# Kernel optimization log

Measured on AMD Instinct MI355X. Metric: run time of the kernel, lower is better.

The kernel has to match this reference:

```python
import jax, jax.numpy as jnp
import numpy as np

N_NODES = 100000
IN_CH, HID_CH, OUT_CH = 128, 128, 64
N_EDGES = 1600000


def setup_inputs() -> dict:
    key = jax.random.key(0)
    ks = jax.random.split(key, 6)
    x = jax.random.normal(ks[0], (N_NODES, IN_CH), dtype=jnp.float32)
    edge_index = jax.random.randint(ks[1], (2, N_EDGES), 0, N_NODES, dtype=jnp.int64)
    # Glorot-style init for GCNConv linear weights, zero bias (PyG defaults)
    s1 = (6.0 / (IN_CH + HID_CH)) ** 0.5
    s2 = (6.0 / (HID_CH + OUT_CH)) ** 0.5
    W1 = jax.random.uniform(ks[2], (IN_CH, HID_CH), jnp.float32, -s1, s1)
    b1 = jnp.zeros((HID_CH,), jnp.float32)
    W2 = jax.random.uniform(ks[3], (HID_CH, OUT_CH), jnp.float32, -s2, s2)
    b2 = jnp.zeros((OUT_CH,), jnp.float32)
    return {"x": x, "W1": W1, "b1": b1, "W2": W2, "b2": b2, "edge_index": edge_index}


def _gcn_norm(edge_index, num_nodes):
    # Add self-loops, compute symmetric normalization deg^{-1/2} A_hat deg^{-1/2}
    loop = jnp.arange(num_nodes, dtype=edge_index.dtype)
    row = jnp.concatenate([edge_index[0], loop])  # source
    col = jnp.concatenate([edge_index[1], loop])  # target
    deg = jax.ops.segment_sum(jnp.ones_like(col, dtype=jnp.float32), col,
                              num_segments=num_nodes)
    dinv = jnp.where(deg > 0, jax.lax.rsqrt(deg), 0.0)
    norm = dinv[row] * dinv[col]  # [E + N]
    return row, col, norm


def _gcn_conv(x, W, b, row, col, norm, num_nodes):
    h = x @ W                              # [N, C_out]
    msg = h[row] * norm[:, None]           # gather over sources, [E+N, C_out]
    out = jax.ops.segment_sum(msg, col, num_segments=num_nodes)  # scatter-add
    return out + b


def reference(x, W1, b1, W2, b2, edge_index):
    num_nodes = x.shape[0]
    row, col, norm = _gcn_norm(edge_index, num_nodes)
    # dropout(p=0.5) in eval mode is identity
    h = _gcn_conv(x, W1, b1, row, col, norm, num_nodes)
    h = jax.nn.relu(h)
    out = _gcn_conv(h, W2, b2, row, col, norm, num_nodes)
    return out
```

## Files before the change

### kernel.cpp

```cpp
#include <hip/hip_runtime.h>
#include <hip/hip_fp16.h>

typedef _Float16 half8 __attribute__((ext_vector_type(8)));
typedef float floatx4 __attribute__((ext_vector_type(4)));
typedef unsigned int uintx4 __attribute__((ext_vector_type(4)));


#define NBUK 128
#define CAPB 16384

__global__ __launch_bounds__(256) void bucket_kernel(const int* __restrict__ rows,
                                                     const int* __restrict__ cols,
                                                     int E, int NSUB,
                                                     int* __restrict__ bcur,
                                                     unsigned* __restrict__ bdata) {
    __shared__ int hcnt[NBUK];
    __shared__ int hbase[NBUK];
    const int tid = threadIdx.x;
    const int chunk0 = blockIdx.x * 2048;
    if (tid < NBUK) hcnt[tid] = 0;
    __syncthreads();
    unsigned up[8];
    int ub[8];
#pragma unroll
    for (int q = 0; q < 8; ++q) {
        int e = chunk0 + q * 256 + tid;
        ub[q] = -1;
        if (e < E) {
            unsigned r = (unsigned)rows[e];
            unsigned c = (unsigned)cols[e];
            int b = (int)(c / (unsigned)NSUB);
            unsigned lc = c - (unsigned)b * (unsigned)NSUB;
            ub[q] = b;
            up[q] = r | (lc << 17);
            atomicAdd(&hcnt[b], 1);
        }
    }
    __syncthreads();
    if (tid < NBUK) {
        hbase[tid] = atomicAdd(&bcur[tid], hcnt[tid]);
        hcnt[tid] = 0;
    }
    __syncthreads();
#pragma unroll
    for (int q = 0; q < 8; ++q) {
        if (ub[q] >= 0) {
            int idx = hbase[ub[q]] + atomicAdd(&hcnt[ub[q]], 1);
            if (idx < CAPB) bdata[(size_t)ub[q] * CAPB + idx] = up[q];
        }
    }
}

__global__ __launch_bounds__(128) void exscan_bucket_kernel(const int* __restrict__ bcur,
                                                            int* __restrict__ bbase,
                                                            int N, int* __restrict__ baseOut) {
    __shared__ int s[NBUK];
    int tid = threadIdx.x;
    int v = min(bcur[tid], CAPB);
    s[tid] = v;
    __syncthreads();
    for (int d = 1; d < NBUK; d <<= 1) {
        int t = (tid >= d) ? s[tid - d] : 0;
        __syncthreads();
        s[tid] += t;
        __syncthreads();
    }
    bbase[tid] = s[tid] - v;
    if (tid == NBUK - 1) baseOut[N] = s[tid];
}

__global__ __launch_bounds__(256) void sortfill_kernel(const unsigned* __restrict__ bdata,
                                                       const int* __restrict__ bcur,
                                                       const int* __restrict__ bbase,
                                                       int NSUB, int N,
                                                       int* __restrict__ baseOut,
                                                       float* __restrict__ dinvOut,
                                                       int* __restrict__ srcSorted) {
    __shared__ int cnt[1024];
    __shared__ int cur[1024];
    __shared__ int wsum[4];
    __shared__ int srcOut[CAPB];
    const int tid = threadIdx.x;
    const int b = blockIdx.x;
    const int nb = min(bcur[b], CAPB);
    const int base0 = bbase[b];
    const int n0 = b * NSUB;
    const int nn = min(NSUB, N - n0);
    const unsigned* bd = bdata + (size_t)b * CAPB;

    for (int i = tid; i < 1024; i += 256) cnt[i] = 0;
    __syncthreads();
    for (int i = tid; i < nb; i += 256) atomicAdd(&cnt[bd[i] >> 17], 1);
    __syncthreads();
    int a0 = cnt[4 * tid], a1 = cnt[4 * tid + 1], a2 = cnt[4 * tid + 2], a3 = cnt[4 * tid + 3];
    int s0 = a0, s1 = s0 + a1, s2 = s1 + a2, s3 = s2 + a3;
    int tot = s3;
    const int lane = tid & 63, wid = tid >> 6;
    for (int off = 1; off < 64; off <<= 1) {
        int u = __shfl_up(tot, off, 64);
        if (lane >= off) tot += u;
    }
    if (lane == 63) wsum[wid] = tot;
    __syncthreads();
    int woff = 0;
#pragma unroll
    for (int w = 0; w < 4; ++w)
        if (w < wid) woff += wsum[w];
    const int tbase = woff + tot - s3;
    cur[4 * tid]     = tbase;
    cur[4 * tid + 1] = tbase + s0;
    cur[4 * tid + 2] = tbase + s1;
    cur[4 * tid + 3] = tbase + s2;
    __syncthreads();
    for (int i = tid; i < nn; i += 256) {
        baseOut[n0 + i] = base0 + cur[i];
        dinvOut[n0 + i] = rsqrtf((float)cnt[i] + 1.0f);
    }
    __syncthreads();
    for (int i = tid; i < nb; i += 256) {
        unsigned u = bd[i];
        int c = (int)(u >> 17);
        int p = atomicAdd(&cur[c], 1);
        srcOut[p] = (int)(u & 0x1FFFFu);
    }
    __syncthreads();
    for (int i = tid; i < nb; i += 256) srcSorted[base0 + i] = srcOut[i];
}

__global__ __launch_bounds__(256) void wtrans_kernel(const float* __restrict__ W,
                                                     __half* __restrict__ WT, int C) {
    int idx = blockIdx.x * 256 + threadIdx.x;
    if (idx >= 128 * C) return;
    int k = idx / C, c = idx % C;
    float v = W[idx];
    WT[c * 128 + (k ^ ((c & 7) << 3))] = __float2half_rn(v);
}

template <int COLS, typename XT>
__global__ __launch_bounds__(256) void mfma_gemm(const XT* __restrict__ X,
                                                 const __half* __restrict__ WT,
                                                 const float* __restrict__ dinv,
                                                 __half* __restrict__ H, int N) {
    __shared__ _Float16 sX[64 * 128];
    __shared__ _Float16 sW[COLS * 128];
    const int tid = threadIdx.x;
    const int row0 = blockIdx.x * 64;

    {
        const uintx4* src = (const uintx4*)WT;
        uintx4* dst = (uintx4*)sW;
        for (int i = tid; i < COLS * 16; i += 256) dst[i] = src[i];
    }
    for (int cidx = tid; cidx < 1024; cidx += 256) {
        int r = cidx >> 4, k8 = cidx & 15;
        int gr = row0 + r;
        half8 h;
#pragma unroll
        for (int q = 0; q < 8; ++q) h[q] = (_Float16)0.f;
        if (gr < N) {
            if constexpr (sizeof(XT) == 4) {
                const float4* p = (const float4*)((const float*)X + (size_t)gr * 128 + k8 * 8);
                float4 f0 = p[0], f1 = p[1];
                h[0] = (_Float16)f0.x; h[1] = (_Float16)f0.y;
                h[2] = (_Float16)f0.z; h[3] = (_Float16)f0.w;
                h[4] = (_Float16)f1.x; h[5] = (_Float16)f1.y;
                h[6] = (_Float16)f1.z; h[7] = (_Float16)f1.w;
            } else {
                h = *(const half8*)((const _Float16*)X + (size_t)gr * 128 + k8 * 8);
            }
        }
        *(half8*)(sX + r * 128 + ((k8 * 8) ^ ((r & 7) << 3))) = h;
    }
    __syncthreads();

    const int w = tid >> 6;
    const int lane = tid & 63;
    const int l15 = lane & 15, l4 = lane >> 4;
    constexpr int WCOLS = COLS / 2;
    constexpr int NCB = WCOLS / 16;
    const int wr = (w >> 1) * 32;
    const int wc = (w & 1) * WCOLS;

    half8 a[2][4];
#pragma unroll
    for (int rb = 0; rb < 2; ++rb) {
        int r = wr + rb * 16 + l15;
#pragma unroll
        for (int kb = 0; kb < 4; ++kb)
            a[rb][kb] = *(const half8*)(sX + r * 128 + ((kb * 32 + l4 * 8) ^ ((r & 7) << 3)));
    }

    floatx4 acc[2][NCB];
#pragma unroll
    for (int rb = 0; rb < 2; ++rb)
#pragma unroll
        for (int cb = 0; cb < NCB; ++cb) acc[rb][cb] = (floatx4)(0.f);

#pragma unroll
    for (int cb = 0; cb < NCB; ++cb) {
        int c = wc + cb * 16 + l15;
#pragma unroll
        for (int kb = 0; kb < 4; ++kb) {
            half8 b = *(const half8*)(sW + c * 128 + ((kb * 32 + l4 * 8) ^ ((c & 7) << 3)));
#pragma unroll
            for (int rb = 0; rb < 2; ++rb)
                acc[rb][cb] = __builtin_amdgcn_mfma_f32_16x16x32_f16(a[rb][kb], b, acc[rb][cb], 0, 0, 0);
        }
    }

#pragma unroll
    for (int rb = 0; rb < 2; ++rb) {
        float dv[4];
#pragma unroll
        for (int r = 0; r < 4; ++r) {
            int gr = row0 + wr + rb * 16 + l4 * 4 + r;
            dv[r] = (gr < N) ? dinv[gr] : 0.f;
        }
#pragma unroll
        for (int cb = 0; cb < NCB; ++cb)
#pragma unroll
            for (int r = 0; r < 4; ++r) {
                int gr = row0 + wr + rb * 16 + l4 * 4 + r;
                if (gr < N) {
                    int gc = wc + cb * 16 + l15;
                    H[(size_t)gr * COLS + gc] = __float2half_rn(acc[rb][cb][r] * dv[r]);
                }
            }
    }
}

__device__ inline void add8(float (&a)[8], uintx4 v) {
    union { uintx4 u; __half2 h[4]; } cv;
    cv.u = v;
#pragma unroll
    for (int q = 0; q < 4; ++q) {
        a[2 * q]     += __low2float(cv.h[q]);
        a[2 * q + 1] += __high2float(cv.h[q]);
    }
}

template <int C, bool RELU, typename OT>
__global__ __launch_bounds__(256) void agg_kernel(const __half* __restrict__ H16,
                                                  const int* __restrict__ srcSorted,
                                                  const int* __restrict__ base,
                                                  const float* __restrict__ dinv,
                                                  const float* __restrict__ b,
                                                  OT* __restrict__ out, int N) {
    constexpr int G = C / 8;
    constexpr int NPB = 256 / G;
    const int lane = threadIdx.x % G;
    const int sub = threadIdx.x / G;
    const int n = blockIdx.x * NPB + sub;
    if (n >= N) return;

    const uintx4* H4 = (const uintx4*)H16;
    const int s = base[n];
    const int e = base[n + 1];

    float acc[8];
#pragma unroll
    for (int q = 0; q < 8; ++q) acc[q] = 0.f;

    int i = s;
    for (; i + 3 < e; i += 4) {
        int s0 = srcSorted[i], s1 = srcSorted[i + 1];
        int s2 = srcSorted[i + 2], s3 = srcSorted[i + 3];
        uintx4 v0 = H4[(size_t)s0 * G + lane];
        uintx4 v1 = H4[(size_t)s1 * G + lane];
        uintx4 v2 = H4[(size_t)s2 * G + lane];
        uintx4 v3 = H4[(size_t)s3 * G + lane];
        add8(acc, v0);
        add8(acc, v1);
        add8(acc, v2);
        add8(acc, v3);
    }
    for (; i < e; ++i) {
        int s0 = srcSorted[i];
        add8(acc, H4[(size_t)s0 * G + lane]);
    }

    const float dn = dinv[n];
    uintx4 hv = H4[(size_t)n * G + lane];
    union { uintx4 u; __half2 h[4]; } cv;
    cv.u = hv;
    float o[8];
#pragma unroll
    for (int q = 0; q < 4; ++q) {
        o[2 * q]     = dn * (acc[2 * q]     + __low2float(cv.h[q]));
        o[2 * q + 1] = dn * (acc[2 * q + 1] + __high2float(cv.h[q]));
    }
    const float4 bb0 = ((const float4*)b)[lane * 2];
    const float4 bb1 = ((const float4*)b)[lane * 2 + 1];
    o[0] += bb0.x; o[1] += bb0.y; o[2] += bb0.z; o[3] += bb0.w;
    o[4] += bb1.x; o[5] += bb1.y; o[6] += bb1.z; o[7] += bb1.w;
    if (RELU) {
#pragma unroll
        for (int q = 0; q < 8; ++q) o[q] = fmaxf(o[q], 0.f);
    }
    if constexpr (sizeof(OT) == 2) {
        half8 st;
#pragma unroll
        for (int q = 0; q < 8; ++q) st[q] = (_Float16)o[q];
        *(half8*)((_Float16*)out + (size_t)n * C + lane * 8) = st;
    } else {
        float4* op = (float4*)((float*)out + (size_t)n * C + lane * 8);
        op[0] = make_float4(o[0], o[1], o[2], o[3]);
        op[1] = make_float4(o[4], o[5], o[6], o[7]);
    }
}

static inline int cdiv(long long a, long long b) { return (int)((a + b - 1) / b); }

extern "C" void kernel_launch(void* const* d_in, const int* in_sizes, int n_in,
                              void* d_out, int out_size, void* d_ws, size_t ws_size,
                              hipStream_t stream) {
    const float* x  = (const float*)d_in[0];
    const float* W1 = (const float*)d_in[1];
    const float* b1 = (const float*)d_in[2];
    const float* W2 = (const float*)d_in[3];
    const float* b2 = (const float*)d_in[4];
    const int*   ei = (const int*)d_in[5];

    const int N = in_sizes[0] / 128;
    const int E = in_sizes[5] / 2;
    const int* rows = ei;
    const int* cols = ei + E;

    const int NSUB = cdiv(N, NBUK);

    char* ws = (char*)d_ws;
    size_t off = 0;
    auto alloc = [&](size_t bytes) {
        size_t p = off;
        off = (off + bytes + 255) & ~(size_t)255;
        return p;
    };
    int*      bcur  = (int*)(ws + alloc((size_t)NBUK * 4));
    int*      bbase = (int*)(ws + alloc((size_t)NBUK * 4));
    int*      base  = (int*)(ws + alloc((size_t)(N + 1) * 4));
    float*    dinv  = (float*)(ws + alloc((size_t)N * 4));
    int*      srcS  = (int*)(ws + alloc((size_t)E * 4));
    unsigned* bdata = (unsigned*)(ws + alloc((size_t)NBUK * CAPB * 4));
    __half*   WT1   = (__half*)(ws + alloc((size_t)128 * 128 * 2));
    __half*   WT2   = (__half*)(ws + alloc((size_t)128 * 64 * 2));
    __half*   H16   = (__half*)(ws + alloc((size_t)N * 128 * 2));
    __half*   X2h   = (__half*)(ws + alloc((size_t)N * 128 * 2));
    (void)ws_size;

    float* OUT = (float*)d_out;

    hipMemsetAsync(bcur, 0, (size_t)NBUK * 4, stream);
    bucket_kernel<<<cdiv(E, 2048), 256, 0, stream>>>(rows, cols, E, NSUB, bcur, bdata);
    exscan_bucket_kernel<<<1, NBUK, 0, stream>>>(bcur, bbase, N, base);
    sortfill_kernel<<<NBUK, 256, 0, stream>>>(bdata, bcur, bbase, NSUB, N, base, dinv, srcS);

    wtrans_kernel<<<cdiv(128 * 128, 256), 256, 0, stream>>>(W1, WT1, 128);
    wtrans_kernel<<<cdiv(128 * 64, 256), 256, 0, stream>>>(W2, WT2, 64);

    mfma_gemm<128, float><<<cdiv(N, 64), 256, 0, stream>>>(x, WT1, dinv, H16, N);
    agg_kernel<128, true, __half><<<cdiv(N, 16), 256, 0, stream>>>(H16, srcS, base, dinv, b1, X2h, N);

    mfma_gemm<64, _Float16><<<cdiv(N, 64), 256, 0, stream>>>((const _Float16*)X2h, WT2, dinv, H16, N);
    agg_kernel<64, false, float><<<cdiv(N, 32), 256, 0, stream>>>(H16, srcS, base, dinv, b2, OUT, N);
}
```

Baseline: 283.9 us.

## Fuse layer-1 aggregation with layer-2 GEMM and pad bucket counters

Layer-1 aggregation (bias, ReLU) now writes a 64-row tile into swizzled shared memory, and the second MFMA GEMM runs on it directly inside one kernel. This removes the N×128 fp16 intermediate write and re-read plus one launch. The gather loop is also unrolled to 8 neighbours, bucket counters are padded to spread global atomics, and bucket blocks handle twice as many edges. In exchange the fused kernel uses 32KB of shared memory and fewer threads per node (16 lanes), which may lower occupancy for the gather phase.

```diff
diff --git a/kernel.cpp b/kernel.cpp
--- a/kernel.cpp
+++ b/kernel.cpp
@@ -8,6 +8,7 @@
 
 #define NBUK 128
 #define CAPB 16384
+#define BPAD 16
 
 __global__ __launch_bounds__(256) void bucket_kernel(const int* __restrict__ rows,
                                                      const int* __restrict__ cols,
@@ -17,13 +18,13 @@
     __shared__ int hcnt[NBUK];
     __shared__ int hbase[NBUK];
     const int tid = threadIdx.x;
-    const int chunk0 = blockIdx.x * 2048;
+    const int chunk0 = blockIdx.x * 4096;
     if (tid < NBUK) hcnt[tid] = 0;
     __syncthreads();
-    unsigned up[8];
-    int ub[8];
-#pragma unroll
-    for (int q = 0; q < 8; ++q) {
+    unsigned up[16];
+    int ub[16];
+#pragma unroll
+    for (int q = 0; q < 16; ++q) {
         int e = chunk0 + q * 256 + tid;
         ub[q] = -1;
         if (e < E) {
@@ -38,12 +39,12 @@
     }
     __syncthreads();
     if (tid < NBUK) {
-        hbase[tid] = atomicAdd(&bcur[tid], hcnt[tid]);
+        hbase[tid] = atomicAdd(&bcur[tid * BPAD], hcnt[tid]);
         hcnt[tid] = 0;
     }
     __syncthreads();
 #pragma unroll
-    for (int q = 0; q < 8; ++q) {
+    for (int q = 0; q < 16; ++q) {
         if (ub[q] >= 0) {
             int idx = hbase[ub[q]] + atomicAdd(&hcnt[ub[q]], 1);
             if (idx < CAPB) bdata[(size_t)ub[q] * CAPB + idx] = up[q];
@@ -56,7 +57,7 @@
                                                             int N, int* __restrict__ baseOut) {
     __shared__ int s[NBUK];
     int tid = threadIdx.x;
-    int v = min(bcur[tid], CAPB);
+    int v = min(bcur[tid * BPAD], CAPB);
     s[tid] = v;
     __syncthreads();
     for (int d = 1; d < NBUK; d <<= 1) {
@@ -82,7 +83,7 @@
     __shared__ int srcOut[CAPB];
     const int tid = threadIdx.x;
     const int b = blockIdx.x;
-    const int nb = min(bcur[b], CAPB);
+    const int nb = min(bcur[b * BPAD], CAPB);
     const int base0 = bbase[b];
     const int n0 = b * NSUB;
     const int nn = min(NSUB, N - n0);
@@ -239,74 +240,172 @@
     }
 }
 
-template <int C, bool RELU, typename OT>
-__global__ __launch_bounds__(256) void agg_kernel(const __half* __restrict__ H16,
-                                                  const int* __restrict__ srcSorted,
-                                                  const int* __restrict__ base,
-                                                  const float* __restrict__ dinv,
-                                                  const float* __restrict__ b,
-                                                  OT* __restrict__ out, int N) {
-    constexpr int G = C / 8;
-    constexpr int NPB = 256 / G;
+template <int G>
+__device__ inline void gather_sum(const uintx4* __restrict__ H4,
+                                  const int* __restrict__ srcSorted,
+                                  int s, int e, int lane, float (&acc)[8]) {
+    int i = s;
+    for (; i + 7 < e; i += 8) {
+        int idx[8];
+#pragma unroll
+        for (int q = 0; q < 8; ++q) idx[q] = srcSorted[i + q];
+        uintx4 v[8];
+#pragma unroll
+        for (int q = 0; q < 8; ++q) v[q] = H4[(size_t)idx[q] * G + lane];
+#pragma unroll
+        for (int q = 0; q < 8; ++q) add8(acc, v[q]);
+    }
+    for (; i + 3 < e; i += 4) {
+        int idx[4];
+#pragma unroll
+        for (int q = 0; q < 4; ++q) idx[q] = srcSorted[i + q];
+        uintx4 v[4];
+#pragma unroll
+        for (int q = 0; q < 4; ++q) v[q] = H4[(size_t)idx[q] * G + lane];
+#pragma unroll
+        for (int q = 0; q < 4; ++q) add8(acc, v[q]);
+    }
+    for (; i < e; ++i) add8(acc, H4[(size_t)srcSorted[i] * G + lane]);
+}
+
+__global__ __launch_bounds__(256) void agg_gemm_kernel(const __half* __restrict__ H16,
+                                                       const int* __restrict__ srcSorted,
+                                                       const int* __restrict__ base,
+                                                       const float* __restrict__ dinv,
+                                                       const float* __restrict__ b1,
+                                                       const __half* __restrict__ WT2,
+                                                       __half* __restrict__ H2, int N) {
+    __shared__ _Float16 sX[64 * 128];
+    __shared__ _Float16 sW[64 * 128];
+    const int tid = threadIdx.x;
+    const int row0 = blockIdx.x * 64;
+
+    {
+        const uintx4* src = (const uintx4*)WT2;
+        uintx4* dst = (uintx4*)sW;
+        for (int i = tid; i < 64 * 16; i += 256) dst[i] = src[i];
+    }
+
+    const int lane16 = tid & 15;
+    const int sub = tid >> 4;
+    const uintx4* H4 = (const uintx4*)H16;
+    const float4 bb0 = ((const float4*)b1)[lane16 * 2];
+    const float4 bb1 = ((const float4*)b1)[lane16 * 2 + 1];
+
+#pragma unroll
+    for (int rnd = 0; rnd < 4; ++rnd) {
+        const int r = rnd * 16 + sub;
+        const int n = row0 + r;
+        float o[8];
+#pragma unroll
+        for (int q = 0; q < 8; ++q) o[q] = 0.f;
+        if (n < N) {
+            float acc[8];
+#pragma unroll
+            for (int q = 0; q < 8; ++q) acc[q] = 0.f;
+            gather_sum<16>(H4, srcSorted, base[n], base[n + 1], lane16, acc);
+            add8(acc, H4[(size_t)n * 16 + lane16]);
+            const float dn = dinv[n];
+            o[0] = fmaxf(dn * acc[0] + bb0.x, 0.f);
+            o[1] = fmaxf(dn * acc[1] + bb0.y, 0.f);
+            o[2] = fmaxf(dn * acc[2] + bb0.z, 0.f);
+            o[3] = fmaxf(dn * acc[3] + bb0.w, 0.f);
+            o[4] = fmaxf(dn * acc[4] + bb1.x, 0.f);
+            o[5] = fmaxf(dn * acc[5] + bb1.y, 0.f);
+            o[6] = fmaxf(dn * acc[6] + bb1.z, 0.f);
+            o[7] = fmaxf(dn * acc[7] + bb1.w, 0.f);
+        }
+        half8 h;
+#pragma unroll
+        for (int q = 0; q < 8; ++q) h[q] = (_Float16)o[q];
+        *(half8*)(sX + r * 128 + ((lane16 * 8) ^ ((r & 7) << 3))) = h;
+    }
+    __syncthreads();
+
+    const int w = tid >> 6;
+    const int lane = tid & 63;
+    const int l15 = lane & 15, l4 = lane >> 4;
+    const int wr = (w >> 1) * 32;
+    const int wc = (w & 1) * 32;
+
+    half8 a[2][4];
+#pragma unroll
+    for (int rb = 0; rb < 2; ++rb) {
+        int r = wr + rb * 16 + l15;
+#pragma unroll
+        for (int kb = 0; kb < 4; ++kb)
+            a[rb][kb] = *(const half8*)(sX + r * 128 + ((kb * 32 + l4 * 8) ^ ((r & 7) << 3)));
+    }
+
+    floatx4 acc[2][2];
+#pragma unroll
+    for (int rb = 0; rb < 2; ++rb)
+#pragma unroll
+        for (int cb = 0; cb < 2; ++cb) acc[rb][cb] = (floatx4)(0.f);
+
+#pragma unroll
+    for (int cb = 0; cb < 2; ++cb) {
+        int c = wc + cb * 16 + l15;
+#pragma unroll
+        for (int kb = 0; kb < 4; ++kb) {
+            half8 b = *(const half8*)(sW + c * 128 + ((kb * 32 + l4 * 8) ^ ((c & 7) << 3)));
+#pragma unroll
+            for (int rb = 0; rb < 2; ++rb)
+                acc[rb][cb] = __builtin_amdgcn_mfma_f32_16x16x32_f16(a[rb][kb], b, acc[rb][cb], 0, 0, 0);
+        }
+    }
+
+#pragma unroll
+    for (int rb = 0; rb < 2; ++rb) {
+        float dv[4];
+#pragma unroll
+        for (int r = 0; r < 4; ++r) {
+            int gr = row0 + wr + rb * 16 + l4 * 4 + r;
+            dv[r] = (gr < N) ? dinv[gr] : 0.f;
+        }
+#pragma unroll
+        for (int cb = 0; cb < 2; ++cb)
+#pragma unroll
+            for (int r = 0; r < 4; ++r) {
+                int gr = row0 + wr + rb * 16 + l4 * 4 + r;
+                if (gr < N) {
+                    int gc = wc + cb * 16 + l15;
+                    H2[(size_t)gr * 64 + gc] = __float2half_rn(acc[rb][cb][r] * dv[r]);
+                }
+            }
+    }
+}
+
+__global__ __launch_bounds__(256) void agg_final_kernel(const __half* __restrict__ H16,
+                                                        const int* __restrict__ srcSorted,
+                                                        const int* __restrict__ base,
+                                                        const float* __restrict__ dinv,
+                                                        const float* __restrict__ b,
+                                                        float* __restrict__ out, int N) {
+    constexpr int G = 8;
     const int lane = threadIdx.x % G;
     const int sub = threadIdx.x / G;
-    const int n = blockIdx.x * NPB + sub;
+    const int n = blockIdx.x * 32 + sub;
     if (n >= N) return;
 
     const uintx4* H4 = (const uintx4*)H16;
-    const int s = base[n];
-    const int e = base[n + 1];
-
     float acc[8];
 #pragma unroll
     for (int q = 0; q < 8; ++q) acc[q] = 0.f;
-
-    int i = s;
-    for (; i + 3 < e; i += 4) {
-        int s0 = srcSorted[i], s1 = srcSorted[i + 1];
-        int s2 = srcSorted[i + 2], s3 = srcSorted[i + 3];
-        uintx4 v0 = H4[(size_t)s0 * G + lane];
-        uintx4 v1 = H4[(size_t)s1 * G + lane];
-        uintx4 v2 = H4[(size_t)s2 * G + lane];
-        uintx4 v3 = H4[(size_t)s3 * G + lane];
-        add8(acc, v0);
-        add8(acc, v1);
-        add8(acc, v2);
-        add8(acc, v3);
-    }
-    for (; i < e; ++i) {
-        int s0 = srcSorted[i];
-        add8(acc, H4[(size_t)s0 * G + lane]);
-    }
+    gather_sum<G>(H4, srcSorted, base[n], base[n + 1], lane, acc);
+    add8(acc, H4[(size_t)n * G + lane]);
 
     const float dn = dinv[n];
-    uintx4 hv = H4[(size_t)n * G + lane];
-    union { uintx4 u; __half2 h[4]; } cv;
-    cv.u = hv;
-    float o[8];
-#pragma unroll
-    for (int q = 0; q < 4; ++q) {
-        o[2 * q]     = dn * (acc[2 * q]     + __low2float(cv.h[q]));
-        o[2 * q + 1] = dn * (acc[2 * q + 1] + __high2float(cv.h[q]));
-    }
     const float4 bb0 = ((const float4*)b)[lane * 2];
     const float4 bb1 = ((const float4*)b)[lane * 2 + 1];
+    float o[8];
+#pragma unroll
+    for (int q = 0; q < 8; ++q) o[q] = dn * acc[q];
     o[0] += bb0.x; o[1] += bb0.y; o[2] += bb0.z; o[3] += bb0.w;
     o[4] += bb1.x; o[5] += bb1.y; o[6] += bb1.z; o[7] += bb1.w;
-    if (RELU) {
-#pragma unroll
-        for (int q = 0; q < 8; ++q) o[q] = fmaxf(o[q], 0.f);
-    }
-    if constexpr (sizeof(OT) == 2) {
-        half8 st;
-#pragma unroll
-        for (int q = 0; q < 8; ++q) st[q] = (_Float16)o[q];
-        *(half8*)((_Float16*)out + (size_t)n * C + lane * 8) = st;
-    } else {
-        float4* op = (float4*)((float*)out + (size_t)n * C + lane * 8);
-        op[0] = make_float4(o[0], o[1], o[2], o[3]);
-        op[1] = make_float4(o[4], o[5], o[6], o[7]);
-    }
+    float4* op = (float4*)(out + (size_t)n * 64 + lane * 8);
+    op[0] = make_float4(o[0], o[1], o[2], o[3]);
+    op[1] = make_float4(o[4], o[5], o[6], o[7]);
 }
 
 static inline int cdiv(long long a, long long b) { return (int)((a + b - 1) / b); }
@@ -335,7 +434,7 @@
         off = (off + bytes + 255) & ~(size_t)255;
         return p;
     };
-    int*      bcur  = (int*)(ws + alloc((size_t)NBUK * 4));
+    int*      bcur  = (int*)(ws + alloc((size_t)NBUK * BPAD * 4));
     int*      bbase = (int*)(ws + alloc((size_t)NBUK * 4));
     int*      base  = (int*)(ws + alloc((size_t)(N + 1) * 4));
     float*    dinv  = (float*)(ws + alloc((size_t)N * 4));
@@ -344,13 +443,13 @@
     __half*   WT1   = (__half*)(ws + alloc((size_t)128 * 128 * 2));
     __half*   WT2   = (__half*)(ws + alloc((size_t)128 * 64 * 2));
     __half*   H16   = (__half*)(ws + alloc((size_t)N * 128 * 2));
-    __half*   X2h   = (__half*)(ws + alloc((size_t)N * 128 * 2));
+    __half*   H2    = (__half*)(ws + alloc((size_t)N * 64 * 2));
     (void)ws_size;
 
     float* OUT = (float*)d_out;
 
-    hipMemsetAsync(bcur, 0, (size_t)NBUK * 4, stream);
-    bucket_kernel<<<cdiv(E, 2048), 256, 0, stream>>>(rows, cols, E, NSUB, bcur, bdata);
+    hipMemsetAsync(bcur, 0, (size_t)NBUK * BPAD * 4, stream);
+    bucket_kernel<<<cdiv(E, 4096), 256, 0, stream>>>(rows, cols, E, NSUB, bcur, bdata);
     exscan_bucket_kernel<<<1, NBUK, 0, stream>>>(bcur, bbase, N, base);
     sortfill_kernel<<<NBUK, 256, 0, stream>>>(bdata, bcur, bbase, NSUB, N, base, dinv, srcS);
 
@@ -358,8 +457,8 @@
     wtrans_kernel<<<cdiv(128 * 64, 256), 256, 0, stream>>>(W2, WT2, 64);
 
     mfma_gemm<128, float><<<cdiv(N, 64), 256, 0, stream>>>(x, WT1, dinv, H16, N);
-    agg_kernel<128, true, __half><<<cdiv(N, 16), 256, 0, stream>>>(H16, srcS, base, dinv, b1, X2h, N);
-
-    mfma_gemm<64, _Float16><<<cdiv(N, 64), 256, 0, stream>>>((const _Float16*)X2h, WT2, dinv, H16, N);
-    agg_kernel<64, false, float><<<cdiv(N, 32), 256, 0, stream>>>(H16, srcS, base, dinv, b2, OUT, N);
-}
+
+    agg_gemm_kernel<<<cdiv(N, 64), 256, 0, stream>>>(H16, srcS, base, dinv, b1, WT2, H2, N);
+
+    agg_final_kernel<<<cdiv(N, 32), 256, 0, stream>>>(H2, srcS, base, dinv, b2, OUT, N);
+}
```

Result: faster. 278.1 us (-2.0%).
